# Kernel tuning notes

Measured on AMD Instinct MI355X. Metric: run time of the kernel, lower is better.

The kernel has to match this reference:

```python
import jax, jax.numpy as jnp
import numpy as np

NUM_GROUPS = 8
GROUP_SIZE = 512
FEATURE_DIM = NUM_GROUPS * GROUP_SIZE
MIN_BITS, MAX_BITS, TARGET_BITS = 2.0, 4.0 * 2, 4.0  # min=2, max=8, target=4
BIT_LEVELS = jnp.array([2.0, 4.0, 8.0], dtype=jnp.float32)
LN_EPS = 1e-5


def setup_inputs() -> dict:
    key = jax.random.key(0)
    ks = jax.random.split(key, 10)
    B, T = 16, 2048
    H = NUM_GROUPS * 2  # hidden of bit predictor
    inv8 = 1.0 / np.sqrt(NUM_GROUPS)
    invH = 1.0 / np.sqrt(H)
    return {
        "importance_scores": jax.random.normal(ks[0], (B, T, FEATURE_DIM), jnp.float32),
        "u": jax.random.uniform(ks[1], (B, NUM_GROUPS), jnp.float32),
        "W1": jax.random.uniform(ks[2], (NUM_GROUPS, H), jnp.float32, -inv8, inv8),
        "b1": jax.random.uniform(ks[3], (H,), jnp.float32, -inv8, inv8),
        "ln_g": jnp.ones((H,), jnp.float32),
        "ln_b": jnp.zeros((H,), jnp.float32),
        "W2": jax.random.uniform(ks[4], (H, NUM_GROUPS), jnp.float32, -invH, invH),
        "b2": jax.random.uniform(ks[5], (NUM_GROUPS,), jnp.float32, -invH, invH),
        "bit_embeddings": jax.random.normal(ks[6], (3, GROUP_SIZE), jnp.float32),
    }


def reference(importance_scores, u, W1, b1, ln_g, ln_b, W2, b2, bit_embeddings):
    B = importance_scores.shape[0]
    # [B,T,D] -> [B,D] -> group means [B,G]
    imp = importance_scores.mean(axis=1)
    group_imp = imp.reshape(B, NUM_GROUPS, GROUP_SIZE).mean(axis=-1)

    # tiny MLP bit predictor: Linear -> GELU -> LayerNorm -> Linear
    h = group_imp @ W1 + b1
    h = jax.nn.gelu(h, approximate=False)
    mu = h.mean(axis=-1, keepdims=True)
    var = ((h - mu) ** 2).mean(axis=-1, keepdims=True)
    h = (h - mu) * jax.lax.rsqrt(var + LN_EPS) * ln_g + ln_b
    logits = h @ W2 + b2

    # training-mode Gumbel perturbation (temperature = 1.0)
    gumbel = -jnp.log(-jnp.log(u + 1e-8) + 1e-8)
    bit_probs = jax.nn.softmax(logits + gumbel, axis=-1)

    # constrained continuous allocation
    alloc = MIN_BITS + bit_probs * (MAX_BITS - MIN_BITS)
    budget = TARGET_BITS * NUM_GROUPS
    alloc = alloc * (budget / alloc.sum(axis=-1, keepdims=True))
    alloc = jnp.clip(alloc, MIN_BITS, MAX_BITS)

    # discretize to nearest bit level with straight-through gradient
    dist = jnp.abs(alloc[..., None] - BIT_LEVELS)  # [B,G,3]
    idx = jnp.argmin(dist, axis=-1)
    hard = BIT_LEVELS[idx]
    discrete_bits = hard + alloc - jax.lax.stop_gradient(alloc)  # value == hard

    # per-group soft codebook mix: softmax(exp(-|b - level|)) @ embeddings
    bit_w = jax.nn.softmax(jnp.exp(-jnp.abs(discrete_bits[..., None] - BIT_LEVELS)), axis=-1)
    embeddings = jnp.einsum("bgl,ld->bgd", bit_w, bit_embeddings)

    group_indices = jnp.broadcast_to(
        (jnp.arange(FEATURE_DIM) // GROUP_SIZE)[None, :], (B, FEATURE_DIM)
    )
    bitrate_loss = (discrete_bits.mean() - TARGET_BITS) ** 2
    diversity_bonus = -(bit_probs * jnp.log(bit_probs + 1e-8)).sum(axis=-1).mean()
    return (discrete_bits, group_indices, embeddings, bitrate_loss, diversity_bonus, bit_probs)
```

## Files before the change

### kernel.cpp

```cpp
#include <hip/hip_runtime.h>
#include <math.h>

#define B_DIM 16
#define T_DIM 2048
#define D_DIM 4096
#define G_DIM 8
#define GS    512
#define H_DIM 16
#define CHUNKS 128
#define NPARTIAL (B_DIM * G_DIM * CHUNKS)

#define OUT_DBITS   0
#define OUT_GIDX    128
#define OUT_EMB     65664
#define OUT_BLOSS   131200
#define OUT_DIV     131201
#define OUT_BPROBS  131202

__global__ __launch_bounds__(256) void k_reduce(const float* __restrict__ scores,
                                                double* __restrict__ partials) {
    const int bid   = blockIdx.x;
    const int b     = bid >> 7;
    const int chunk = bid & 127;
    const int tid   = threadIdx.x;

    const float4* base = reinterpret_cast<const float4*>(
        scores + (size_t)b * T_DIM * D_DIM + (size_t)chunk * 16 * D_DIM);

    double a0 = 0.0, a1 = 0.0, a2 = 0.0, a3 = 0.0;
    #pragma unroll 4
    for (int r = 0; r < 16; ++r) {
        const float4* row = base + (size_t)r * (D_DIM / 4);
        const float4 v0 = row[tid];
        const float4 v1 = row[tid + 256];
        const float4 v2 = row[tid + 512];
        const float4 v3 = row[tid + 768];
        a0 += (double)v0.x + (double)v0.y + (double)v0.z + (double)v0.w;
        a1 += (double)v1.x + (double)v1.y + (double)v1.z + (double)v1.w;
        a2 += (double)v2.x + (double)v2.y + (double)v2.z + (double)v2.w;
        a3 += (double)v3.x + (double)v3.y + (double)v3.z + (double)v3.w;
    }

    const int lane = tid & 63;
    const int wave = tid >> 6;
    __shared__ double wsum[4][4];
    double acc[4] = {a0, a1, a2, a3};
    #pragma unroll
    for (int p = 0; p < 4; ++p) {
        double v = acc[p];
        #pragma unroll
        for (int off = 32; off > 0; off >>= 1) v += __shfl_down(v, off, 64);
        if (lane == 0) wsum[wave][p] = v;
    }
    __syncthreads();

    if (tid < G_DIM) {
        const int p  = tid >> 1;
        const int w0 = (tid & 1) * 2;
        partials[(size_t)(b * G_DIM + tid) * CHUNKS + chunk] = wsum[w0][p] + wsum[w0 + 1][p];
    }
}

__global__ __launch_bounds__(128) void k_mlp(const double* __restrict__ partials,
                                             const float* __restrict__ u,
                                             const float* __restrict__ W1,
                                             const float* __restrict__ b1,
                                             const float* __restrict__ ln_g,
                                             const float* __restrict__ ln_b,
                                             const float* __restrict__ W2,
                                             const float* __restrict__ b2,
                                             float* __restrict__ out,
                                             float* __restrict__ bitw) {
    __shared__ float gi[B_DIM * G_DIM];
    __shared__ float ent[B_DIM];
    __shared__ float bitsum[B_DIM];
    const int tid = threadIdx.x;

    if (tid < 128) {
        double s = 0.0;
        #pragma unroll
        for (int c = 0; c < CHUNKS; ++c) s += partials[(size_t)tid * CHUNKS + c];
        gi[tid] = (float)(s * (1.0 / ((double)T_DIM * (double)GS)));
    }
    __syncthreads();

    if (tid < B_DIM) {
        const int b = tid;
        float h[H_DIM];
        #pragma unroll
        for (int i = 0; i < H_DIM; ++i) {
            float a = b1[i];
            #pragma unroll
            for (int g = 0; g < G_DIM; ++g) a += gi[b * G_DIM + g] * W1[g * H_DIM + i];
            h[i] = 0.5f * a * (1.0f + erff(a * 0.70710678118654752440f));
        }
        float mu = 0.f;
        #pragma unroll
        for (int i = 0; i < H_DIM; ++i) mu += h[i];
        mu *= (1.0f / (float)H_DIM);
        float var = 0.f;
        #pragma unroll
        for (int i = 0; i < H_DIM; ++i) { float d = h[i] - mu; var += d * d; }
        var *= (1.0f / (float)H_DIM);
        const float inv = rsqrtf(var + 1e-5f);
        #pragma unroll
        for (int i = 0; i < H_DIM; ++i) h[i] = (h[i] - mu) * inv * ln_g[i] + ln_b[i];

        float z[G_DIM];
        #pragma unroll
        for (int j = 0; j < G_DIM; ++j) {
            float a = b2[j];
            #pragma unroll
            for (int i = 0; i < H_DIM; ++i) a += h[i] * W2[i * G_DIM + j];
            const float uu = u[b * G_DIM + j];
            const float gum = -logf(-logf(uu + 1e-8f) + 1e-8f);
            z[j] = a + gum;
        }
        float m = z[0];
        #pragma unroll
        for (int j = 1; j < G_DIM; ++j) m = fmaxf(m, z[j]);
        float p[G_DIM]; float ssum = 0.f;
        #pragma unroll
        for (int j = 0; j < G_DIM; ++j) { p[j] = expf(z[j] - m); ssum += p[j]; }
        const float rs = 1.0f / ssum;

        float alloc[G_DIM]; float asum = 0.f;
        #pragma unroll
        for (int j = 0; j < G_DIM; ++j) {
            p[j] *= rs;
            alloc[j] = 2.0f + p[j] * 6.0f;
            asum += alloc[j];
        }
        const float scale = 32.0f / asum;

        float entb = 0.f, bs = 0.f;
        #pragma unroll
        for (int j = 0; j < G_DIM; ++j) {
            float a = alloc[j] * scale;
            a = fminf(fmaxf(a, 2.0f), 8.0f);
            const float hard = (a <= 3.0f) ? 2.0f : ((a <= 6.0f) ? 4.0f : 8.0f);
            out[OUT_DBITS + b * G_DIM + j]  = hard;
            out[OUT_BPROBS + b * G_DIM + j] = p[j];
            entb += p[j] * logf(p[j] + 1e-8f);
            bs += hard;
            const float x0 = expf(-fabsf(hard - 2.0f));
            const float x1 = expf(-fabsf(hard - 4.0f));
            const float x2 = expf(-fabsf(hard - 8.0f));
            const float mm = fmaxf(x0, fmaxf(x1, x2));
            const float e0 = expf(x0 - mm), e1 = expf(x1 - mm), e2 = expf(x2 - mm);
            const float ir = 1.0f / (e0 + e1 + e2);
            bitw[(b * G_DIM + j) * 3 + 0] = e0 * ir;
            bitw[(b * G_DIM + j) * 3 + 1] = e1 * ir;
            bitw[(b * G_DIM + j) * 3 + 2] = e2 * ir;
        }
        ent[b] = entb;
        bitsum[b] = bs;
    }
    __syncthreads();

    if (tid == 0) {
        float tb = 0.f, te = 0.f;
        #pragma unroll
        for (int b = 0; b < B_DIM; ++b) { tb += bitsum[b]; te += ent[b]; }
        const float mb = tb * (1.0f / (float)(B_DIM * G_DIM));
        out[OUT_BLOSS] = (mb - 4.0f) * (mb - 4.0f);
        out[OUT_DIV]   = -te * (1.0f / (float)B_DIM);
    }
}

__global__ __launch_bounds__(256) void k_emb(const float* __restrict__ bitw,
                                             const float* __restrict__ emb,
                                             float* __restrict__ out) {
    const int l = blockIdx.x * 256 + threadIdx.x;
    const int b   = l >> 10;
    const int rem = l & 1023;
    const int g   = rem >> 7;
    const int j4  = rem & 127;

    const float4* e4 = reinterpret_cast<const float4*>(emb);
    const float4 e0 = e4[0 * 128 + j4];
    const float4 e1 = e4[1 * 128 + j4];
    const float4 e2 = e4[2 * 128 + j4];
    const float w0 = bitw[(b * G_DIM + g) * 3 + 0];
    const float w1 = bitw[(b * G_DIM + g) * 3 + 1];
    const float w2 = bitw[(b * G_DIM + g) * 3 + 2];

    float4 r;
    r.x = w0 * e0.x + w1 * e1.x + w2 * e2.x;
    r.y = w0 * e0.y + w1 * e1.y + w2 * e2.y;
    r.z = w0 * e0.z + w1 * e1.z + w2 * e2.z;
    r.w = w0 * e0.w + w1 * e1.w + w2 * e2.w;

    float4* o4 = reinterpret_cast<float4*>(out);
    o4[(OUT_EMB / 4) + l] = r;

    const float gv = (float)g;
    o4[(OUT_GIDX / 4) + l] = make_float4(gv, gv, gv, gv);
}

extern "C" void kernel_launch(void* const* d_in, const int* in_sizes, int n_in,
                              void* d_out, int out_size, void* d_ws, size_t ws_size,
                              hipStream_t stream) {
    const float* scores = (const float*)d_in[0];
    const float* u      = (const float*)d_in[1];
    const float* W1     = (const float*)d_in[2];
    const float* b1     = (const float*)d_in[3];
    const float* ln_g   = (const float*)d_in[4];
    const float* ln_b   = (const float*)d_in[5];
    const float* W2     = (const float*)d_in[6];
    const float* b2     = (const float*)d_in[7];
    const float* emb    = (const float*)d_in[8];
    float* out = (float*)d_out;

    double* partials = (double*)d_ws;
    float*  bitw     = (float*)((char*)d_ws + NPARTIAL * sizeof(double));

    k_reduce<<<B_DIM * CHUNKS, 256, 0, stream>>>(scores, partials);
    k_mlp<<<1, 128, 0, stream>>>(partials, u, W1, b1, ln_g, ln_b, W2, b2, out, bitw);
    k_emb<<<64, 256, 0, stream>>>(bitw, emb, out);
}
```

Before: 110.1 us.

## Fuse MLP and embedding kernels into one tail kernel; use nontemporal loads

Merges the single-block MLP kernel and the embedding kernel into one 64-block tail kernel. Each block redundantly recomputes its batch's group means and MLP to obtain its bit weights locally, while block 0 also writes the global outputs and losses. This removes one kernel launch and the global round trip for the bit weights, at the cost of duplicated tiny MLP work. The streaming reduction also switches to nontemporal loads to avoid polluting the cache with the 512MB input.

New measurement: 94.90 us. 13.8% less time.

```diff
diff --git a/kernel.cpp b/kernel.cpp
--- a/kernel.cpp
+++ b/kernel.cpp
@@ -17,6 +17,8 @@
 #define OUT_DIV     131201
 #define OUT_BPROBS  131202
 
+typedef float f32x4 __attribute__((ext_vector_type(4)));
+
 __global__ __launch_bounds__(256) void k_reduce(const float* __restrict__ scores,
                                                 double* __restrict__ partials) {
     const int bid   = blockIdx.x;
@@ -24,17 +26,17 @@
     const int chunk = bid & 127;
     const int tid   = threadIdx.x;
 
-    const float4* base = reinterpret_cast<const float4*>(
+    const f32x4* base = reinterpret_cast<const f32x4*>(
         scores + (size_t)b * T_DIM * D_DIM + (size_t)chunk * 16 * D_DIM);
 
     double a0 = 0.0, a1 = 0.0, a2 = 0.0, a3 = 0.0;
     #pragma unroll 4
     for (int r = 0; r < 16; ++r) {
-        const float4* row = base + (size_t)r * (D_DIM / 4);
-        const float4 v0 = row[tid];
-        const float4 v1 = row[tid + 256];
-        const float4 v2 = row[tid + 512];
-        const float4 v3 = row[tid + 768];
+        const f32x4* row = base + (size_t)r * (D_DIM / 4);
+        const f32x4 v0 = __builtin_nontemporal_load(row + tid);
+        const f32x4 v1 = __builtin_nontemporal_load(row + tid + 256);
+        const f32x4 v2 = __builtin_nontemporal_load(row + tid + 512);
+        const f32x4 v3 = __builtin_nontemporal_load(row + tid + 768);
         a0 += (double)v0.x + (double)v0.y + (double)v0.z + (double)v0.w;
         a1 += (double)v1.x + (double)v1.y + (double)v1.z + (double)v1.w;
         a2 += (double)v2.x + (double)v2.y + (double)v2.z + (double)v2.w;
@@ -61,129 +63,172 @@
     }
 }
 
-__global__ __launch_bounds__(128) void k_mlp(const double* __restrict__ partials,
-                                             const float* __restrict__ u,
-                                             const float* __restrict__ W1,
-                                             const float* __restrict__ b1,
-                                             const float* __restrict__ ln_g,
-                                             const float* __restrict__ ln_b,
-                                             const float* __restrict__ W2,
-                                             const float* __restrict__ b2,
-                                             float* __restrict__ out,
-                                             float* __restrict__ bitw) {
-    __shared__ float gi[B_DIM * G_DIM];
-    __shared__ float ent[B_DIM];
-    __shared__ float bitsum[B_DIM];
+__device__ __forceinline__ void run_mlp(const float* __restrict__ gi8, int b,
+                                        const float* __restrict__ u,
+                                        const float* __restrict__ W1,
+                                        const float* __restrict__ b1,
+                                        const float* __restrict__ ln_g,
+                                        const float* __restrict__ ln_b,
+                                        const float* __restrict__ W2,
+                                        const float* __restrict__ b2,
+                                        float* __restrict__ p,
+                                        float* __restrict__ hard,
+                                        float (*bw)[3],
+                                        float* entb_out, float* bs_out) {
+    float h[H_DIM];
+    #pragma unroll
+    for (int i = 0; i < H_DIM; ++i) {
+        float a = b1[i];
+        #pragma unroll
+        for (int g = 0; g < G_DIM; ++g) a += gi8[g] * W1[g * H_DIM + i];
+        h[i] = 0.5f * a * (1.0f + erff(a * 0.70710678118654752440f));
+    }
+    float mu = 0.f;
+    #pragma unroll
+    for (int i = 0; i < H_DIM; ++i) mu += h[i];
+    mu *= (1.0f / (float)H_DIM);
+    float var = 0.f;
+    #pragma unroll
+    for (int i = 0; i < H_DIM; ++i) { float d = h[i] - mu; var += d * d; }
+    var *= (1.0f / (float)H_DIM);
+    const float inv = rsqrtf(var + 1e-5f);
+    #pragma unroll
+    for (int i = 0; i < H_DIM; ++i) h[i] = (h[i] - mu) * inv * ln_g[i] + ln_b[i];
+
+    float z[G_DIM];
+    #pragma unroll
+    for (int j = 0; j < G_DIM; ++j) {
+        float a = b2[j];
+        #pragma unroll
+        for (int i = 0; i < H_DIM; ++i) a += h[i] * W2[i * G_DIM + j];
+        const float uu = u[b * G_DIM + j];
+        z[j] = a + (-logf(-logf(uu + 1e-8f) + 1e-8f));
+    }
+    float m = z[0];
+    #pragma unroll
+    for (int j = 1; j < G_DIM; ++j) m = fmaxf(m, z[j]);
+    float ssum = 0.f;
+    #pragma unroll
+    for (int j = 0; j < G_DIM; ++j) { p[j] = expf(z[j] - m); ssum += p[j]; }
+    const float rs = 1.0f / ssum;
+
+    float alloc[G_DIM]; float asum = 0.f;
+    #pragma unroll
+    for (int j = 0; j < G_DIM; ++j) {
+        p[j] *= rs;
+        alloc[j] = 2.0f + p[j] * 6.0f;
+        asum += alloc[j];
+    }
+    const float scale = 32.0f / asum;
+
+    float entb = 0.f, bs = 0.f;
+    #pragma unroll
+    for (int j = 0; j < G_DIM; ++j) {
+        float a = alloc[j] * scale;
+        a = fminf(fmaxf(a, 2.0f), 8.0f);
+        const float hd = (a <= 3.0f) ? 2.0f : ((a <= 6.0f) ? 4.0f : 8.0f);
+        hard[j] = hd;
+        entb += p[j] * logf(p[j] + 1e-8f);
+        bs += hd;
+        const float x0 = expf(-fabsf(hd - 2.0f));
+        const float x1 = expf(-fabsf(hd - 4.0f));
+        const float x2 = expf(-fabsf(hd - 8.0f));
+        const float mm = fmaxf(x0, fmaxf(x1, x2));
+        const float e0 = expf(x0 - mm), e1 = expf(x1 - mm), e2 = expf(x2 - mm);
+        const float ir = 1.0f / (e0 + e1 + e2);
+        bw[j][0] = e0 * ir;
+        bw[j][1] = e1 * ir;
+        bw[j][2] = e2 * ir;
+    }
+    *entb_out = entb;
+    *bs_out = bs;
+}
+
+__global__ __launch_bounds__(256) void k_tail(const double* __restrict__ partials,
+                                              const float* __restrict__ u,
+                                              const float* __restrict__ W1,
+                                              const float* __restrict__ b1,
+                                              const float* __restrict__ ln_g,
+                                              const float* __restrict__ ln_b,
+                                              const float* __restrict__ W2,
+                                              const float* __restrict__ b2,
+                                              const float* __restrict__ emb,
+                                              float* __restrict__ out) {
+    const int blk = blockIdx.x;
+    const int b   = blk >> 2;
+    const int q   = blk & 3;
     const int tid = threadIdx.x;
 
-    if (tid < 128) {
-        double s = 0.0;
-        #pragma unroll
-        for (int c = 0; c < CHUNKS; ++c) s += partials[(size_t)tid * CHUNKS + c];
-        gi[tid] = (float)(s * (1.0 / ((double)T_DIM * (double)GS)));
+    __shared__ float s_gi[B_DIM * G_DIM];
+    __shared__ float s_w[G_DIM][3];
+    __shared__ float s_ent[B_DIM], s_bs[B_DIM];
+
+    if (blk == 0) {
+        if (tid < 128) {
+            double s = 0.0;
+            #pragma unroll 8
+            for (int c = 0; c < CHUNKS; ++c) s += partials[(size_t)tid * CHUNKS + c];
+            s_gi[tid] = (float)(s * (1.0 / ((double)T_DIM * (double)GS)));
+        }
+        __syncthreads();
+        if (tid < B_DIM) {
+            float p[G_DIM], hard[G_DIM], bw[G_DIM][3], entb, bs;
+            run_mlp(&s_gi[tid * G_DIM], tid, u, W1, b1, ln_g, ln_b, W2, b2,
+                    p, hard, bw, &entb, &bs);
+            #pragma unroll
+            for (int j = 0; j < G_DIM; ++j) {
+                out[OUT_DBITS  + tid * G_DIM + j] = hard[j];
+                out[OUT_BPROBS + tid * G_DIM + j] = p[j];
+            }
+            s_ent[tid] = entb;
+            s_bs[tid]  = bs;
+            if (tid == 0) {
+                #pragma unroll
+                for (int j = 0; j < G_DIM; ++j) {
+                    s_w[j][0] = bw[j][0]; s_w[j][1] = bw[j][1]; s_w[j][2] = bw[j][2];
+                }
+            }
+        }
+        __syncthreads();
+        if (tid == 0) {
+            float tb = 0.f, te = 0.f;
+            #pragma unroll
+            for (int bb = 0; bb < B_DIM; ++bb) { tb += s_bs[bb]; te += s_ent[bb]; }
+            const float mb = tb * (1.0f / (float)(B_DIM * G_DIM));
+            out[OUT_BLOSS] = (mb - 4.0f) * (mb - 4.0f);
+            out[OUT_DIV]   = -te * (1.0f / (float)B_DIM);
+        }
+    } else {
+        const double* pb = partials + (size_t)b * G_DIM * CHUNKS;
+        double v = 0.0;
+        #pragma unroll
+        for (int k = 0; k < 4; ++k) v += pb[tid * 4 + k];
+        #pragma unroll
+        for (int off = 16; off > 0; off >>= 1) v += __shfl_down(v, off, 32);
+        if ((tid & 31) == 0)
+            s_gi[tid >> 5] = (float)(v * (1.0 / ((double)T_DIM * (double)GS)));
+        __syncthreads();
+        if (tid == 0) {
+            float p[G_DIM], hard[G_DIM], bw[G_DIM][3], entb, bs;
+            run_mlp(&s_gi[0], b, u, W1, b1, ln_g, ln_b, W2, b2,
+                    p, hard, bw, &entb, &bs);
+            #pragma unroll
+            for (int j = 0; j < G_DIM; ++j) {
+                s_w[j][0] = bw[j][0]; s_w[j][1] = bw[j][1]; s_w[j][2] = bw[j][2];
+            }
+        }
     }
     __syncthreads();
 
-    if (tid < B_DIM) {
-        const int b = tid;
-        float h[H_DIM];
-        #pragma unroll
-        for (int i = 0; i < H_DIM; ++i) {
-            float a = b1[i];
-            #pragma unroll
-            for (int g = 0; g < G_DIM; ++g) a += gi[b * G_DIM + g] * W1[g * H_DIM + i];
-            h[i] = 0.5f * a * (1.0f + erff(a * 0.70710678118654752440f));
-        }
-        float mu = 0.f;
-        #pragma unroll
-        for (int i = 0; i < H_DIM; ++i) mu += h[i];
-        mu *= (1.0f / (float)H_DIM);
-        float var = 0.f;
-        #pragma unroll
-        for (int i = 0; i < H_DIM; ++i) { float d = h[i] - mu; var += d * d; }
-        var *= (1.0f / (float)H_DIM);
-        const float inv = rsqrtf(var + 1e-5f);
-        #pragma unroll
-        for (int i = 0; i < H_DIM; ++i) h[i] = (h[i] - mu) * inv * ln_g[i] + ln_b[i];
-
-        float z[G_DIM];
-        #pragma unroll
-        for (int j = 0; j < G_DIM; ++j) {
-            float a = b2[j];
-            #pragma unroll
-            for (int i = 0; i < H_DIM; ++i) a += h[i] * W2[i * G_DIM + j];
-            const float uu = u[b * G_DIM + j];
-            const float gum = -logf(-logf(uu + 1e-8f) + 1e-8f);
-            z[j] = a + gum;
-        }
-        float m = z[0];
-        #pragma unroll
-        for (int j = 1; j < G_DIM; ++j) m = fmaxf(m, z[j]);
-        float p[G_DIM]; float ssum = 0.f;
-        #pragma unroll
-        for (int j = 0; j < G_DIM; ++j) { p[j] = expf(z[j] - m); ssum += p[j]; }
-        const float rs = 1.0f / ssum;
-
-        float alloc[G_DIM]; float asum = 0.f;
-        #pragma unroll
-        for (int j = 0; j < G_DIM; ++j) {
-            p[j] *= rs;
-            alloc[j] = 2.0f + p[j] * 6.0f;
-            asum += alloc[j];
-        }
-        const float scale = 32.0f / asum;
-
-        float entb = 0.f, bs = 0.f;
-        #pragma unroll
-        for (int j = 0; j < G_DIM; ++j) {
-            float a = alloc[j] * scale;
-            a = fminf(fmaxf(a, 2.0f), 8.0f);
-            const float hard = (a <= 3.0f) ? 2.0f : ((a <= 6.0f) ? 4.0f : 8.0f);
-            out[OUT_DBITS + b * G_DIM + j]  = hard;
-            out[OUT_BPROBS + b * G_DIM + j] = p[j];
-            entb += p[j] * logf(p[j] + 1e-8f);
-            bs += hard;
-            const float x0 = expf(-fabsf(hard - 2.0f));
-            const float x1 = expf(-fabsf(hard - 4.0f));
-            const float x2 = expf(-fabsf(hard - 8.0f));
-            const float mm = fmaxf(x0, fmaxf(x1, x2));
-            const float e0 = expf(x0 - mm), e1 = expf(x1 - mm), e2 = expf(x2 - mm);
-            const float ir = 1.0f / (e0 + e1 + e2);
-            bitw[(b * G_DIM + j) * 3 + 0] = e0 * ir;
-            bitw[(b * G_DIM + j) * 3 + 1] = e1 * ir;
-            bitw[(b * G_DIM + j) * 3 + 2] = e2 * ir;
-        }
-        ent[b] = entb;
-        bitsum[b] = bs;
-    }
-    __syncthreads();
-
-    if (tid == 0) {
-        float tb = 0.f, te = 0.f;
-        #pragma unroll
-        for (int b = 0; b < B_DIM; ++b) { tb += bitsum[b]; te += ent[b]; }
-        const float mb = tb * (1.0f / (float)(B_DIM * G_DIM));
-        out[OUT_BLOSS] = (mb - 4.0f) * (mb - 4.0f);
-        out[OUT_DIV]   = -te * (1.0f / (float)B_DIM);
-    }
-}
-
-__global__ __launch_bounds__(256) void k_emb(const float* __restrict__ bitw,
-                                             const float* __restrict__ emb,
-                                             float* __restrict__ out) {
-    const int l = blockIdx.x * 256 + threadIdx.x;
-    const int b   = l >> 10;
-    const int rem = l & 1023;
-    const int g   = rem >> 7;
-    const int j4  = rem & 127;
+    const int l  = blk * 256 + tid;
+    const int g  = q * 2 + (tid >> 7);
+    const int j4 = tid & 127;
 
     const float4* e4 = reinterpret_cast<const float4*>(emb);
     const float4 e0 = e4[0 * 128 + j4];
     const float4 e1 = e4[1 * 128 + j4];
     const float4 e2 = e4[2 * 128 + j4];
-    const float w0 = bitw[(b * G_DIM + g) * 3 + 0];
-    const float w1 = bitw[(b * G_DIM + g) * 3 + 1];
-    const float w2 = bitw[(b * G_DIM + g) * 3 + 2];
+    const float w0 = s_w[g][0], w1 = s_w[g][1], w2 = s_w[g][2];
 
     float4 r;
     r.x = w0 * e0.x + w1 * e1.x + w2 * e2.x;
@@ -213,9 +258,7 @@
     float* out = (float*)d_out;
 
     double* partials = (double*)d_ws;
-    float*  bitw     = (float*)((char*)d_ws + NPARTIAL * sizeof(double));
 
     k_reduce<<<B_DIM * CHUNKS, 256, 0, stream>>>(scores, partials);
-    k_mlp<<<1, 128, 0, stream>>>(partials, u, W1, b1, ln_g, ln_b, W2, b2, out, bitw);
-    k_emb<<<64, 256, 0, stream>>>(bitw, emb, out);
-}
+    k_tail<<<64, 256, 0, stream>>>(partials, u, W1, b1, ln_g, ln_b, W2, b2, emb, out);
+}
```
